# Optimization experiments

Measured on AMD Instinct MI355X. Metric: run time of the kernel, lower is better.

The kernel has to match this reference:

```python
import jax, jax.numpy as jnp
import numpy as np

N = 8_388_608      # query points (e.g., 2048x4096 texture)
RES_UP = 224       # grid1 2D table resolution (from init solver)
RES_DN = 8         # grid0 3D table resolution (from init solver)
LATENT = 3


def nonlin(t):
    # periodic non-linearity: wrap learned table values into [0,1)
    # (normalize=True in SpatialGrid2D/3D)
    return t - jnp.floor(t)


def bilinear2d(x, table):
    # x: (N,2) in [0,1); table: (U,V,L)
    U, V, _ = table.shape
    u = x[:, 0] * (U - 1)
    v = x[:, 1] * (V - 1)
    u0 = jnp.clip(jnp.floor(u), 0, U - 2).astype(jnp.int32)
    v0 = jnp.clip(jnp.floor(v), 0, V - 2).astype(jnp.int32)
    fu = (u - u0)[:, None]
    fv = (v - v0)[:, None]
    c00 = table[u0, v0]
    c01 = table[u0, v0 + 1]
    c10 = table[u0 + 1, v0]
    c11 = table[u0 + 1, v0 + 1]
    c0 = c00 * (1 - fv) + c01 * fv
    c1 = c10 * (1 - fv) + c11 * fv
    return c0 * (1 - fu) + c1 * fu  # (N, L)


def trilinear3d(x, table):
    # x: (N,3) in [0,1); table: (U,V,W,L)
    U, V, W, _ = table.shape
    u = x[:, 0] * (U - 1)
    v = x[:, 1] * (V - 1)
    w = x[:, 2] * (W - 1)
    u0 = jnp.clip(jnp.floor(u), 0, U - 2).astype(jnp.int32)
    v0 = jnp.clip(jnp.floor(v), 0, V - 2).astype(jnp.int32)
    w0 = jnp.clip(jnp.floor(w), 0, W - 2).astype(jnp.int32)
    fu = (u - u0)[:, None]
    fv = (v - v0)[:, None]
    fw = (w - w0)[:, None]
    c000 = table[u0, v0, w0]
    c001 = table[u0, v0, w0 + 1]
    c010 = table[u0, v0 + 1, w0]
    c011 = table[u0, v0 + 1, w0 + 1]
    c100 = table[u0 + 1, v0, w0]
    c101 = table[u0 + 1, v0, w0 + 1]
    c110 = table[u0 + 1, v0 + 1, w0]
    c111 = table[u0 + 1, v0 + 1, w0 + 1]
    c00 = c000 * (1 - fw) + c001 * fw
    c01 = c010 * (1 - fw) + c011 * fw
    c10 = c100 * (1 - fw) + c101 * fw
    c11 = c110 * (1 - fw) + c111 * fw
    c0 = c00 * (1 - fv) + c01 * fv
    c1 = c10 * (1 - fv) + c11 * fv
    return c0 * (1 - fu) + c1 * fu  # (N, L)


def setup_inputs() -> dict:
    key = jax.random.key(0)
    k1, k2, k3 = jax.random.split(key, 3)
    x = jax.random.uniform(k1, (N, 2), dtype=jnp.float32)
    table2d = jax.random.uniform(k2, (RES_UP, RES_UP, LATENT), dtype=jnp.float32)
    table3d = jax.random.uniform(k3, (RES_DN, RES_DN, RES_DN, LATENT), dtype=jnp.float32)
    return {"x": x, "table2d": table2d, "table3d": table3d}


def reference(x, table2d, table3d):
    # forward: grid0(grid1(x)) -- 2D bilinear lookup feeding a 3D trilinear lookup
    key = bilinear2d(x, nonlin(table2d))       # (N,3) coordinates into 3D grid
    out = trilinear3d(key, nonlin(table3d))    # (N,3)
    return out
```

## Files before the change

### kernel.cpp

```cpp
#include <hip/hip_runtime.h>

#define RES_UP 224
#define RES_DN 8
#define T2D_N (RES_UP * RES_UP)
#define T3D_N (RES_DN * RES_DN * RES_DN)

__device__ __forceinline__ float fracf(float t) { return t - floorf(t); }

__device__ __forceinline__ uint32_t q3w(const float* p) {
    uint32_t q0 = (uint32_t)(fracf(p[0]) * 1023.0f + 0.5f);
    uint32_t q1 = (uint32_t)(fracf(p[1]) * 1023.0f + 0.5f);
    uint32_t q2 = (uint32_t)(fracf(p[2]) * 1023.0f + 0.5f);
    return q0 | (q1 << 10) | (q2 << 20);
}

__global__ __launch_bounds__(256) void repack2d_q(const float* __restrict__ t2d,
                                                  uint4* __restrict__ pk) {
    int i = blockIdx.x * blockDim.x + threadIdx.x;
    if (i >= T2D_N) return;
    int u = i / RES_UP;
    int v = i - u * RES_UP;
    int un = min(u + 1, RES_UP - 1);
    int vn = min(v + 1, RES_UP - 1);
    uint4 t;
    t.x = q3w(t2d + ((size_t)u  * RES_UP + v ) * 3);
    t.y = q3w(t2d + ((size_t)u  * RES_UP + vn) * 3);
    t.z = q3w(t2d + ((size_t)un * RES_UP + v ) * 3);
    t.w = q3w(t2d + ((size_t)un * RES_UP + vn) * 3);
    pk[i] = t;
}

__global__ __launch_bounds__(256) void repack3d_q(const float* __restrict__ t3d,
                                                  uint4* __restrict__ pk3) {
    int i = blockIdx.x * blockDim.x + threadIdx.x;
    if (i >= T3D_N) return;
    int a = i >> 6, b = (i >> 3) & 7, c = i & 7;
    int an = min(a + 1, 7), bn = min(b + 1, 7), cn = min(c + 1, 7);
    uint4 A, B;
    uint32_t* Aw = &A.x;
    uint32_t* Bw = &B.x;
    #pragma unroll
    for (int l = 0; l < 3; ++l) {
        uint32_t a00 = (uint32_t)(fracf(t3d[(((a  * 8) + b ) * 8 + c ) * 3 + l]) * 255.0f + 0.5f);
        uint32_t a01 = (uint32_t)(fracf(t3d[(((a  * 8) + b ) * 8 + cn) * 3 + l]) * 255.0f + 0.5f);
        uint32_t a10 = (uint32_t)(fracf(t3d[(((a  * 8) + bn) * 8 + c ) * 3 + l]) * 255.0f + 0.5f);
        uint32_t a11 = (uint32_t)(fracf(t3d[(((a  * 8) + bn) * 8 + cn) * 3 + l]) * 255.0f + 0.5f);
        uint32_t b00 = (uint32_t)(fracf(t3d[(((an * 8) + b ) * 8 + c ) * 3 + l]) * 255.0f + 0.5f);
        uint32_t b01 = (uint32_t)(fracf(t3d[(((an * 8) + b ) * 8 + cn) * 3 + l]) * 255.0f + 0.5f);
        uint32_t b10 = (uint32_t)(fracf(t3d[(((an * 8) + bn) * 8 + c ) * 3 + l]) * 255.0f + 0.5f);
        uint32_t b11 = (uint32_t)(fracf(t3d[(((an * 8) + bn) * 8 + cn) * 3 + l]) * 255.0f + 0.5f);
        Aw[l] = a00 | (a01 << 8) | (a10 << 16) | (a11 << 24);
        Bw[l] = b00 | (b01 << 8) | (b10 << 16) | (b11 << 24);
    }
    A.w = 0; B.w = 0;
    pk3[i] = A;
    pk3[i + T3D_N] = B;
}

__device__ __forceinline__ float uq10(uint32_t w, int s) {
    return (float)((w >> s) & 1023u);
}
__device__ __forceinline__ float ub(uint32_t w, int k) {
    return (float)((w >> (k * 8)) & 255u);
}

__global__ __launch_bounds__(256) void fused_main_q(
    const float* __restrict__ x,
    const uint4* __restrict__ t2,
    const uint4* __restrict__ t3p,
    float* __restrict__ out,
    int nquad)
{
    __shared__ uint4 s3[2 * T3D_N];

    #pragma unroll
    for (int i = threadIdx.x; i < 2 * T3D_N; i += 256) {
        s3[i] = t3p[i];
    }
    __syncthreads();

    int q = blockIdx.x * blockDim.x + threadIdx.x;
    if (q >= nquad) return;

    const float4 xa = ((const float4*)x)[q * 2 + 0];
    const float4 xb = ((const float4*)x)[q * 2 + 1];
    const float px[4] = {xa.x, xa.z, xb.x, xb.z};
    const float py[4] = {xa.y, xa.w, xb.y, xb.w};

    int   idx[4];
    float fu[4], fv[4];
    #pragma unroll
    for (int k = 0; k < 4; ++k) {
        float u = px[k] * (float)(RES_UP - 1);
        float v = py[k] * (float)(RES_UP - 1);
        int u0 = (int)u;
        int v0 = (int)v;
        fu[k] = u - (float)u0;
        fv[k] = v - (float)v0;
        idx[k] = u0 * RES_UP + v0;
    }

    uint4 g[4];
    #pragma unroll
    for (int k = 0; k < 4; ++k) g[k] = t2[idx[k]];

    int   sidx[4];
    float fa[4], fb[4], fc[4];
    #pragma unroll
    for (int k = 0; k < 4; ++k) {
        const float S = (float)(RES_DN - 1) / 1023.0f;
        float wu0 = 1.0f - fu[k], wv0 = 1.0f - fv[k];
        float r00 = wu0 * wv0, r01 = wu0 * fv[k];
        float r10 = fu[k] * wv0, r11 = fu[k] * fv[k];
        float key[3];
        #pragma unroll
        for (int l = 0; l < 3; ++l) {
            int s = l * 10;
            float d = uq10(g[k].x, s) * r00;
            d = fmaf(uq10(g[k].y, s), r01, d);
            d = fmaf(uq10(g[k].z, s), r10, d);
            d = fmaf(uq10(g[k].w, s), r11, d);
            key[l] = d * S;
        }
        int a0 = min((int)key[0], RES_DN - 2);
        int b0 = min((int)key[1], RES_DN - 2);
        int c0 = min((int)key[2], RES_DN - 2);
        fa[k] = key[0] - (float)a0;
        fb[k] = key[1] - (float)b0;
        fc[k] = key[2] - (float)c0;
        sidx[k] = (a0 * RES_DN + b0) * RES_DN + c0;
    }

    uint4 qA[4], qB[4];
    #pragma unroll
    for (int k = 0; k < 4; ++k) {
        qA[k] = s3[sidx[k]];
        qB[k] = s3[sidx[k] + T3D_N];
    }

    float res[12];
    #pragma unroll
    for (int k = 0; k < 4; ++k) {
        const float D = 1.0f / 255.0f;
        float wb0 = 1.0f - fb[k], wc0 = 1.0f - fc[k];
        float q00 = wb0 * wc0, q01 = wb0 * fc[k];
        float q10 = fb[k] * wc0, q11 = fb[k] * fc[k];
        float wa0 = 1.0f - fa[k];
        const uint32_t* Aw = &qA[k].x;
        const uint32_t* Bw = &qB[k].x;
        #pragma unroll
        for (int l = 0; l < 3; ++l) {
            uint32_t wA = Aw[l], wB = Bw[l];
            float dA = ub(wA, 0) * q00;
            dA = fmaf(ub(wA, 1), q01, dA);
            dA = fmaf(ub(wA, 2), q10, dA);
            dA = fmaf(ub(wA, 3), q11, dA);
            float dB = ub(wB, 0) * q00;
            dB = fmaf(ub(wB, 1), q01, dB);
            dB = fmaf(ub(wB, 2), q10, dB);
            dB = fmaf(ub(wB, 3), q11, dB);
            res[k * 3 + l] = (wa0 * dA + fa[k] * dB) * D;
        }
    }

    float4* o = (float4*)(out + (size_t)q * 12);
    o[0] = make_float4(res[0], res[1], res[2],  res[3]);
    o[1] = make_float4(res[4], res[5], res[6],  res[7]);
    o[2] = make_float4(res[8], res[9], res[10], res[11]);
}

__device__ __forceinline__ float4 lerp4(const float4 a, const float4 b, const float t) {
    const float s = 1.0f - t;
    return make_float4(a.x * s + b.x * t, a.y * s + b.y * t, a.z * s + b.z * t, 0.0f);
}

__global__ __launch_bounds__(256) void fused_fallback(
    const float* __restrict__ x,
    const float* __restrict__ t2d,
    const float* __restrict__ t3d,
    float* __restrict__ out,
    int nquad)
{
    __shared__ float4 s3d[T3D_N];
    for (int i = threadIdx.x; i < T3D_N; i += blockDim.x) {
        float a = t3d[i * 3 + 0];
        float b = t3d[i * 3 + 1];
        float c = t3d[i * 3 + 2];
        s3d[i] = make_float4(fracf(a), fracf(b), fracf(c), 0.0f);
    }
    __syncthreads();

    const int stride = gridDim.x * blockDim.x;
    for (int q = blockIdx.x * blockDim.x + threadIdx.x; q < nquad; q += stride) {
        const float4 xa = ((const float4*)x)[q * 2 + 0];
        const float4 xb = ((const float4*)x)[q * 2 + 1];
        const float px[4] = {xa.x, xa.z, xb.x, xb.z};
        const float py[4] = {xa.y, xa.w, xb.y, xb.w};
        float res[12];

        #pragma unroll
        for (int k = 0; k < 4; ++k) {
            float u = px[k] * (float)(RES_UP - 1);
            float v = py[k] * (float)(RES_UP - 1);
            int u0 = min(max((int)floorf(u), 0), RES_UP - 2);
            int v0 = min(max((int)floorf(v), 0), RES_UP - 2);
            float fuu = u - (float)u0;
            float fvv = v - (float)v0;

            const float* p00 = t2d + ((size_t)u0 * RES_UP + v0) * 3;
            const float* p10 = p00 + RES_UP * 3;
            float key[3];
            #pragma unroll
            for (int l = 0; l < 3; ++l) {
                float c00 = fracf(p00[l]);
                float c01 = fracf(p00[3 + l]);
                float c10 = fracf(p10[l]);
                float c11 = fracf(p10[3 + l]);
                float c0 = c00 * (1.0f - fvv) + c01 * fvv;
                float c1 = c10 * (1.0f - fvv) + c11 * fvv;
                key[l] = c0 * (1.0f - fuu) + c1 * fuu;
            }

            float uu = key[0] * (float)(RES_DN - 1);
            float vv = key[1] * (float)(RES_DN - 1);
            float ww = key[2] * (float)(RES_DN - 1);
            int a0 = min(max((int)floorf(uu), 0), RES_DN - 2);
            int b0 = min(max((int)floorf(vv), 0), RES_DN - 2);
            int c0 = min(max((int)floorf(ww), 0), RES_DN - 2);
            float fa = uu - (float)a0;
            float fb = vv - (float)b0;
            float fc = ww - (float)c0;

            int sidx = (a0 * RES_DN + b0) * RES_DN + c0;
            float4 e00 = lerp4(s3d[sidx], s3d[sidx + 1], fc);
            float4 e01 = lerp4(s3d[sidx + RES_DN], s3d[sidx + RES_DN + 1], fc);
            float4 e10 = lerp4(s3d[sidx + 64], s3d[sidx + 65], fc);
            float4 e11 = lerp4(s3d[sidx + 72], s3d[sidx + 73], fc);
            float4 e = lerp4(lerp4(e00, e01, fb), lerp4(e10, e11, fb), fa);

            res[k * 3 + 0] = e.x;
            res[k * 3 + 1] = e.y;
            res[k * 3 + 2] = e.z;
        }

        float4* o = (float4*)(out + (size_t)q * 12);
        o[0] = make_float4(res[0], res[1], res[2],  res[3]);
        o[1] = make_float4(res[4], res[5], res[6],  res[7]);
        o[2] = make_float4(res[8], res[9], res[10], res[11]);
    }
}

extern "C" void kernel_launch(void* const* d_in, const int* in_sizes, int n_in,
                              void* d_out, int out_size, void* d_ws, size_t ws_size,
                              hipStream_t stream) {
    const float* x   = (const float*)d_in[0];
    const float* t2d = (const float*)d_in[1];
    const float* t3d = (const float*)d_in[2];
    float* out = (float*)d_out;

    int npts  = in_sizes[0] / 2;
    int nquad = npts / 4;

    const size_t need = (size_t)(T2D_N + 2 * T3D_N) * sizeof(uint4);
    if (ws_size >= need) {
        uint4* ws2 = (uint4*)d_ws;
        uint4* ws3 = ws2 + T2D_N;
        repack2d_q<<<(T2D_N + 255) / 256, 256, 0, stream>>>(t2d, ws2);
        repack3d_q<<<(T3D_N + 255) / 256, 256, 0, stream>>>(t3d, ws3);
        fused_main_q<<<(nquad + 255) / 256, 256, 0, stream>>>(x, ws2, ws3, out, nquad);
    } else {
        fused_fallback<<<2048, 256, 0, stream>>>(x, t2d, t3d, out, nquad);
    }
}
```

Baseline: 68.87 us.

## Add software-pipelined persistent kernel overlapping x loads, table gathers and compute

Adds a fused_pipe kernel in which each of 2048x256 threads handles four quads. The loads of x and the 2D table gathers for the next quad are issued while the current quad is finished, and x is read with nontemporal loads. It is dispatched only when nquad equals exactly 4*nth, which is true for N=8M, and otherwise falls back to the old kernel. The goal is to hide gather latency through ILP instead of relying on occupancy, at the cost of higher register pressure. The old kernel is also restructured to interleave the shared-memory lookups with compute.

```diff
diff --git a/kernel.cpp b/kernel.cpp
--- a/kernel.cpp
+++ b/kernel.cpp
@@ -4,6 +4,8 @@
 #define RES_DN 8
 #define T2D_N (RES_UP * RES_UP)
 #define T3D_N (RES_DN * RES_DN * RES_DN)
+
+typedef float floatx4 __attribute__((ext_vector_type(4)));
 
 __device__ __forceinline__ float fracf(float t) { return t - floorf(t); }
 
@@ -64,6 +66,121 @@
     return (float)((w >> (k * 8)) & 255u);
 }
 
+__global__ __launch_bounds__(256) void fused_pipe(
+    const float* __restrict__ x,
+    const uint4* __restrict__ t2,
+    const uint4* __restrict__ t3p,
+    float* __restrict__ out,
+    int nth)
+{
+    __shared__ uint4 s3[2 * T3D_N];
+    #pragma unroll
+    for (int i = threadIdx.x; i < 2 * T3D_N; i += 256) s3[i] = t3p[i];
+    __syncthreads();
+
+    const int tid = blockIdx.x * 256 + threadIdx.x;
+
+    floatx4 xA0, xA1, xB0, xB1;
+    float fuA[4], fvA[4]; uint4 gA[4];
+    float fuB[4], fvB[4]; uint4 gB[4];
+
+#define LOADX(X0, X1, it) do {                                                  \
+    const floatx4* _p = (const floatx4*)(x + ((size_t)tid + (size_t)(it) * nth) * 8); \
+    X0 = __builtin_nontemporal_load(_p);                                        \
+    X1 = __builtin_nontemporal_load(_p + 1);                                    \
+} while (0)
+
+#define ADDR(X0, X1, FU, FV, G) do {                                            \
+    float _px[4] = {X0.x, X0.z, X1.x, X1.z};                                    \
+    float _py[4] = {X0.y, X0.w, X1.y, X1.w};                                    \
+    _Pragma("unroll")                                                           \
+    for (int k = 0; k < 4; ++k) {                                               \
+        float _u = _px[k] * (float)(RES_UP - 1);                                \
+        float _v = _py[k] * (float)(RES_UP - 1);                                \
+        int _u0 = (int)_u;                                                      \
+        int _v0 = (int)_v;                                                      \
+        FU[k] = _u - (float)_u0;                                                \
+        FV[k] = _v - (float)_v0;                                                \
+        G[k] = t2[_u0 * RES_UP + _v0];                                          \
+    }                                                                           \
+} while (0)
+
+#define FIN(FU, FV, G, it) do {                                                 \
+    float _res[12];                                                             \
+    _Pragma("unroll")                                                           \
+    for (int k = 0; k < 4; ++k) {                                               \
+        const float _S = (float)(RES_DN - 1) / 1023.0f;                         \
+        float _wu0 = 1.0f - FU[k], _wv0 = 1.0f - FV[k];                         \
+        float _r00 = _wu0 * _wv0,  _r01 = _wu0 * FV[k];                         \
+        float _r10 = FU[k] * _wv0, _r11 = FU[k] * FV[k];                        \
+        float _key[3];                                                          \
+        _Pragma("unroll")                                                       \
+        for (int l = 0; l < 3; ++l) {                                           \
+            int _s = l * 10;                                                    \
+            float _d = uq10(G[k].x, _s) * _r00;                                 \
+            _d = fmaf(uq10(G[k].y, _s), _r01, _d);                              \
+            _d = fmaf(uq10(G[k].z, _s), _r10, _d);                              \
+            _d = fmaf(uq10(G[k].w, _s), _r11, _d);                              \
+            _key[l] = _d * _S;                                                  \
+        }                                                                       \
+        int _a0 = min((int)_key[0], RES_DN - 2);                                \
+        int _b0 = min((int)_key[1], RES_DN - 2);                                \
+        int _c0 = min((int)_key[2], RES_DN - 2);                                \
+        float _fa = _key[0] - (float)_a0;                                       \
+        float _fb = _key[1] - (float)_b0;                                       \
+        float _fc = _key[2] - (float)_c0;                                       \
+        int _si = (_a0 * RES_DN + _b0) * RES_DN + _c0;                          \
+        uint4 _qA = s3[_si];                                                    \
+        uint4 _qB = s3[_si + T3D_N];                                            \
+        const float _D = 1.0f / 255.0f;                                         \
+        float _wb0 = 1.0f - _fb, _wc0 = 1.0f - _fc;                             \
+        float _q00 = _wb0 * _wc0, _q01 = _wb0 * _fc;                            \
+        float _q10 = _fb * _wc0,  _q11 = _fb * _fc;                             \
+        float _wa0 = 1.0f - _fa;                                                \
+        const uint32_t* _Aw = &_qA.x;                                           \
+        const uint32_t* _Bw = &_qB.x;                                           \
+        _Pragma("unroll")                                                       \
+        for (int l = 0; l < 3; ++l) {                                           \
+            uint32_t _wA = _Aw[l], _wB = _Bw[l];                                \
+            float _dA = ub(_wA, 0) * _q00;                                      \
+            _dA = fmaf(ub(_wA, 1), _q01, _dA);                                  \
+            _dA = fmaf(ub(_wA, 2), _q10, _dA);                                  \
+            _dA = fmaf(ub(_wA, 3), _q11, _dA);                                  \
+            float _dB = ub(_wB, 0) * _q00;                                      \
+            _dB = fmaf(ub(_wB, 1), _q01, _dB);                                  \
+            _dB = fmaf(ub(_wB, 2), _q10, _dB);                                  \
+            _dB = fmaf(ub(_wB, 3), _q11, _dB);                                  \
+            _res[k * 3 + l] = (_wa0 * _dA + _fa * _dB) * _D;                    \
+        }                                                                       \
+    }                                                                           \
+    float4* _o = (float4*)(out + ((size_t)tid + (size_t)(it) * nth) * 12);      \
+    _o[0] = make_float4(_res[0], _res[1], _res[2],  _res[3]);                   \
+    _o[1] = make_float4(_res[4], _res[5], _res[6],  _res[7]);                   \
+    _o[2] = make_float4(_res[8], _res[9], _res[10], _res[11]);                  \
+} while (0)
+
+    LOADX(xA0, xA1, 0);
+    LOADX(xB0, xB1, 1);
+    ADDR(xA0, xA1, fuA, fvA, gA);
+
+    LOADX(xA0, xA1, 2);
+    ADDR(xB0, xB1, fuB, fvB, gB);
+    FIN(fuA, fvA, gA, 0);
+
+    LOADX(xB0, xB1, 3);
+    ADDR(xA0, xA1, fuA, fvA, gA);
+    FIN(fuB, fvB, gB, 1);
+
+    ADDR(xB0, xB1, fuB, fvB, gB);
+    FIN(fuA, fvA, gA, 2);
+
+    FIN(fuB, fvB, gB, 3);
+
+#undef LOADX
+#undef ADDR
+#undef FIN
+}
+
 __global__ __launch_bounds__(256) void fused_main_q(
     const float* __restrict__ x,
     const uint4* __restrict__ t2,
@@ -72,11 +189,8 @@
     int nquad)
 {
     __shared__ uint4 s3[2 * T3D_N];
-
-    #pragma unroll
-    for (int i = threadIdx.x; i < 2 * T3D_N; i += 256) {
-        s3[i] = t3p[i];
-    }
+    #pragma unroll
+    for (int i = threadIdx.x; i < 2 * T3D_N; i += 256) s3[i] = t3p[i];
     __syncthreads();
 
     int q = blockIdx.x * blockDim.x + threadIdx.x;
@@ -104,8 +218,7 @@
     #pragma unroll
     for (int k = 0; k < 4; ++k) g[k] = t2[idx[k]];
 
-    int   sidx[4];
-    float fa[4], fb[4], fc[4];
+    float res[12];
     #pragma unroll
     for (int k = 0; k < 4; ++k) {
         const float S = (float)(RES_DN - 1) / 1023.0f;
@@ -125,29 +238,19 @@
         int a0 = min((int)key[0], RES_DN - 2);
         int b0 = min((int)key[1], RES_DN - 2);
         int c0 = min((int)key[2], RES_DN - 2);
-        fa[k] = key[0] - (float)a0;
-        fb[k] = key[1] - (float)b0;
-        fc[k] = key[2] - (float)c0;
-        sidx[k] = (a0 * RES_DN + b0) * RES_DN + c0;
-    }
-
-    uint4 qA[4], qB[4];
-    #pragma unroll
-    for (int k = 0; k < 4; ++k) {
-        qA[k] = s3[sidx[k]];
-        qB[k] = s3[sidx[k] + T3D_N];
-    }
-
-    float res[12];
-    #pragma unroll
-    for (int k = 0; k < 4; ++k) {
+        float fa = key[0] - (float)a0;
+        float fb = key[1] - (float)b0;
+        float fc = key[2] - (float)c0;
+        int si = (a0 * RES_DN + b0) * RES_DN + c0;
+        uint4 qA = s3[si];
+        uint4 qB = s3[si + T3D_N];
         const float D = 1.0f / 255.0f;
-        float wb0 = 1.0f - fb[k], wc0 = 1.0f - fc[k];
-        float q00 = wb0 * wc0, q01 = wb0 * fc[k];
-        float q10 = fb[k] * wc0, q11 = fb[k] * fc[k];
-        float wa0 = 1.0f - fa[k];
-        const uint32_t* Aw = &qA[k].x;
-        const uint32_t* Bw = &qB[k].x;
+        float wb0 = 1.0f - fb, wc0 = 1.0f - fc;
+        float q00 = wb0 * wc0, q01 = wb0 * fc;
+        float q10 = fb * wc0, q11 = fb * fc;
+        float wa0 = 1.0f - fa;
+        const uint32_t* Aw = &qA.x;
+        const uint32_t* Bw = &qB.x;
         #pragma unroll
         for (int l = 0; l < 3; ++l) {
             uint32_t wA = Aw[l], wB = Bw[l];
@@ -159,7 +262,7 @@
             dB = fmaf(ub(wB, 1), q01, dB);
             dB = fmaf(ub(wB, 2), q10, dB);
             dB = fmaf(ub(wB, 3), q11, dB);
-            res[k * 3 + l] = (wa0 * dA + fa[k] * dB) * D;
+            res[k * 3 + l] = (wa0 * dA + fa * dB) * D;
         }
     }
 
@@ -267,7 +370,14 @@
         uint4* ws3 = ws2 + T2D_N;
         repack2d_q<<<(T2D_N + 255) / 256, 256, 0, stream>>>(t2d, ws2);
         repack3d_q<<<(T3D_N + 255) / 256, 256, 0, stream>>>(t3d, ws3);
-        fused_main_q<<<(nquad + 255) / 256, 256, 0, stream>>>(x, ws2, ws3, out, nquad);
+
+        const int grid = 2048;
+        const int nth  = grid * 256;
+        if (nquad == 4 * nth) {
+            fused_pipe<<<grid, 256, 0, stream>>>(x, ws2, ws3, out, nth);
+        } else {
+            fused_main_q<<<(nquad + 255) / 256, 256, 0, stream>>>(x, ws2, ws3, out, nquad);
+        }
     } else {
         fused_fallback<<<2048, 256, 0, stream>>>(x, t2d, t3d, out, nquad);
     }
```

Measured after the change: 98.94 us. 43.6% more time.
